# Performance work log

Measured on AMD Instinct MI355X. Metric: run time of the kernel, lower is better.

## Reference

```python
import jax, jax.numpy as jnp
import numpy as np

N, E, F_IN, E_DIM, H, T, L = 20000, 160000, 64, 32, 100, 5, 2
F_T = H // T  # per-tower output = 20

# PNAConv degree histogram -> average log-degree scalar (constant w.r.t. grads)
DEG_HIST = np.array([7,54,215,574,1147,1835,2447,2797,2797,2486,1989,1446,964,593,339,181,136], dtype=np.float64)
_bins = np.arange(len(DEG_HIST), dtype=np.float64)
AVG_LOG = np.float32((np.log(_bins + 1.0) * DEG_HIST).sum() / DEG_HIST.sum())


def _segment_stats(m, dst, n):
    # m: [E, T, H] messages; returns count [N] and [N, T, 4H] (mean|min|max|std)
    ones = jnp.ones((m.shape[0],), m.dtype)
    cnt = jax.ops.segment_sum(ones, dst, n)
    c = jnp.maximum(cnt, 1.0)[:, None, None]
    mean = jax.ops.segment_sum(m, dst, n) / c
    mean2 = jax.ops.segment_sum(m * m, dst, n) / c
    std = jnp.sqrt(jnp.maximum(mean2 - mean * mean, 0.0) + 1e-5)
    has = (cnt > 0)[:, None, None]
    mn = jnp.where(has, jax.ops.segment_min(m, dst, n), 0.0)
    mx = jnp.where(has, jax.ops.segment_max(m, dst, n), 0.0)
    return cnt, jnp.concatenate([mean, mn, mx, std], -1)


def _pna_conv(x, ea, src, dst, eeW, eeb, preW, preb, postW, postb, linW, linb):
    # x: [N, H] nodes, ea: [E, H] embedded edge attrs
    n = x.shape[0]
    e = ea.shape[0]
    xt = jnp.broadcast_to(x[:, None, :], (n, T, H))            # divide_input=False: repeat per tower
    e_enc = ea @ eeW + eeb                                     # edge_encoder [E, H]
    e_t = jnp.broadcast_to(e_enc[:, None, :], (e, T, H))
    h = jnp.concatenate([xt[dst], xt[src], e_t], -1)           # message cat [x_i, x_j, edge] -> [E, T, 3H]
    m = jnp.einsum('etf,tfh->eth', h, preW) + preb             # per-tower pre-MLP (1 layer) -> [E, T, H]
    cnt, agg = _segment_stats(m, dst, n)                       # [N, T, 4H]
    amp = (jnp.log(jnp.maximum(cnt, 1.0) + 1.0) / AVG_LOG)[:, None, None]
    scaled = jnp.concatenate([agg, agg * amp, agg / amp], -1)  # identity|amplification|attenuation -> [N, T, 12H]
    out = jnp.concatenate([xt, scaled], -1)                    # [N, T, 13H]
    out = jnp.einsum('ntf,tfo->nto', out, postW) + postb       # per-tower post-MLP -> [N, T, H/T]
    return out.reshape(n, H) @ linW + linb


def reference(x, edge_attr, node_emb_W, node_emb_b, edge_emb_W, edge_emb_b,
              ee_W, ee_b, pre_W, pre_b, post_W, post_b, lin_W, lin_b,
              bn_gamma, bn_beta, em_W1, em_b1, em_W2, em_b2,
              mlp_W1, mlp_b1, mlp_W2, mlp_b2, mlp_W3, mlp_b3, edge_index):
    src, dst = edge_index[0], edge_index[1]
    h = x @ node_emb_W + node_emb_b
    ea = edge_attr @ edge_emb_W + edge_emb_b
    for l in range(L):
        c = _pna_conv(h, ea, src, dst, ee_W[l], ee_b[l], pre_W[l], pre_b[l],
                      post_W[l], post_b[l], lin_W[l], lin_b[l])
        mu = c.mean(0)
        var = jnp.mean((c - mu) ** 2, 0)                       # BatchNorm (batch stats, biased var)
        h = jax.nn.relu(bn_gamma[l] * (c - mu) * jax.lax.rsqrt(var + 1e-5) + bn_beta[l])
        z = jnp.concatenate([h[src], h[dst], ea], -1)          # edge-update MLP
        ea = jax.nn.relu(z @ em_W1[l] + em_b1[l]) @ em_W2[l] + em_b2[l]
    o = jnp.concatenate([jax.nn.relu(h[src]), jax.nn.relu(h[dst]), ea], -1)
    o = jax.nn.relu(o @ mlp_W1 + mlp_b1)
    o = jax.nn.relu(o @ mlp_W2 + mlp_b2)
    return o @ mlp_W3 + mlp_b3                                 # [E, 1] per-edge logits


def setup_inputs() -> dict:
    key = jax.random.key(0)
    ks = iter(jax.random.split(key, 40))
    g = lambda shape, fan: jax.random.normal(next(ks), shape, jnp.float32) / np.float32(np.sqrt(fan))
    return {
        'x': jax.random.normal(next(ks), (N, F_IN), jnp.float32),
        'edge_attr': jax.random.normal(next(ks), (E, E_DIM), jnp.float32),
        'node_emb_W': g((F_IN, H), F_IN), 'node_emb_b': jnp.zeros((H,), jnp.float32),
        'edge_emb_W': g((E_DIM, H), E_DIM), 'edge_emb_b': jnp.zeros((H,), jnp.float32),
        'ee_W': g((L, H, H), H), 'ee_b': jnp.zeros((L, H), jnp.float32),
        'pre_W': g((L, T, 3 * H, H), 3 * H), 'pre_b': jnp.zeros((L, T, H), jnp.float32),
        'post_W': g((L, T, 13 * H, F_T), 13 * H), 'post_b': jnp.zeros((L, T, F_T), jnp.float32),
        'lin_W': g((L, H, H), H), 'lin_b': jnp.zeros((L, H), jnp.float32),
        'bn_gamma': jnp.ones((L, H), jnp.float32), 'bn_beta': jnp.zeros((L, H), jnp.float32),
        'em_W1': g((L, 3 * H, H), 3 * H), 'em_b1': jnp.zeros((L, H), jnp.float32),
        'em_W2': g((L, H, H), H), 'em_b2': jnp.zeros((L, H), jnp.float32),
        'mlp_W1': g((3 * H, 50), 3 * H), 'mlp_b1': jnp.zeros((50,), jnp.float32),
        'mlp_W2': g((50, 25), 50), 'mlp_b2': jnp.zeros((25,), jnp.float32),
        'mlp_W3': g((25, 1), 25), 'mlp_b3': jnp.zeros((1,), jnp.float32),
        'edge_index': jax.random.randint(next(ks), (2, E), 0, N, dtype=jnp.int32),
    }
```

## Files before the change

### kernel.cpp

```cpp
#include <hip/hip_runtime.h>
#include <cmath>

#define NN 20000
#define EE 160000
#define HH 100
#define TT 5
#define FT 20
#define LL 2
#define FIN 64
#define EDIM 32
#define CN 2500
#define NCH 8
#define CAP 23040

typedef __attribute__((ext_vector_type(8))) short bf16x8;
typedef __attribute__((ext_vector_type(4))) float f32x4;

__device__ inline float bf2f(unsigned short u) {
    union { unsigned i; float f; } x; x.i = ((unsigned)u) << 16; return x.f;
}
__device__ inline unsigned short f2bf(float f) {
    union { float f; unsigned i; } x; x.f = f;
    unsigned r = x.i + 0x7fff + ((x.i >> 16) & 1);
    return (unsigned short)(r >> 16);
}
__device__ inline unsigned packsplit(float v) {
    unsigned short hi = f2bf(v);
    float rem = v - bf2f(hi);
    unsigned short lo = f2bf(rem);
    return ((unsigned)hi << 16) | lo;
}

__global__ void hist_kernel(const int* __restrict__ edst, int* __restrict__ counts) {
    int e = blockIdx.x * 256 + threadIdx.x;
    if (e < EE) atomicAdd(&counts[edst[e]], 1);
}

__global__ __launch_bounds__(1024) void scan_kernel(const int* __restrict__ counts,
                                                    int* __restrict__ row_ptr,
                                                    int* __restrict__ fillp) {
    __shared__ int part[1024];
    int tid = threadIdx.x;
    const int PER = 20;
    int base = tid * PER;
    int s = 0;
    for (int i = 0; i < PER; ++i) {
        int idx = base + i;
        if (idx < NN) s += counts[idx];
    }
    part[tid] = s;
    __syncthreads();
    for (int off = 1; off < 1024; off <<= 1) {
        int v = (tid >= off) ? part[tid - off] : 0;
        __syncthreads();
        part[tid] += v;
        __syncthreads();
    }
    int run = (tid == 0) ? 0 : part[tid - 1];
    for (int i = 0; i < PER; ++i) {
        int idx = base + i;
        if (idx < NN) {
            row_ptr[idx] = run;
            fillp[idx] = run;
            run += counts[idx];
        }
    }
    if (tid == 1023) row_ptr[NN] = run;
}

__global__ void fill_kernel(const int* __restrict__ edst, int* __restrict__ fillp,
                            int* __restrict__ esorted) {
    int e = blockIdx.x * 256 + threadIdx.x;
    if (e < EE) {
        int pos = atomicAdd(&fillp[edst[e]], 1);
        esorted[pos] = e;
    }
}

__global__ void pack_kernel(const float* __restrict__ src, unsigned* __restrict__ dst, int n) {
    int i = blockIdx.x * 256 + threadIdx.x;
    if (i < n) dst[i] = packsplit(src[i]);
}

__global__ void repack_preW(const float* __restrict__ preW_l, float* __restrict__ Bcat) {
    int idx = blockIdx.x * 256 + threadIdx.x;
    if (idx >= 300 * 500) return;
    int k = idx / 500, n = idx % 500;
    int t = n / 100, hc = n % 100;
    Bcat[idx] = preW_l[(t * 300 + k) * 100 + hc];
}

__global__ void comb_kernel(const float* __restrict__ Bcat, const float* __restrict__ eeW,
                            const float* __restrict__ eeb, const float* __restrict__ preb,
                            float* __restrict__ Bcomb, float* __restrict__ biasc) {
    int idx = blockIdx.x * 256 + threadIdx.x;
    if (idx < 50000) {
        int i = idx / 500, n = idx % 500;
        float acc = 0.f;
        for (int j = 0; j < 100; ++j) acc += eeW[i * 100 + j] * Bcat[(200 + j) * 500 + n];
        Bcomb[idx] = acc;
    } else if (idx < 50500) {
        int n = idx - 50000;
        float acc = preb[n];
        for (int j = 0; j < 100; ++j) acc += eeb[j] * Bcat[(200 + j) * 500 + n];
        biasc[n] = acc;
    }
}

__global__ void pack_BT(const float* __restrict__ src, unsigned* __restrict__ dst,
                        int Kuse, int Nsrc, int koff, int total) {
    int idx = blockIdx.x * 256 + threadIdx.x;
    if (idx >= total) return;
    int n = idx >> 7, k = idx & 127;
    float v = (k < Kuse && n < Nsrc) ? src[(size_t)(koff + k) * Nsrc + n] : 0.f;
    dst[idx] = packsplit(v);
}

__global__ void pack_Wx(const float* __restrict__ postW, unsigned* __restrict__ dst) {
    int idx = blockIdx.x * 256 + threadIdx.x;
    if (idx >= 128 * 128) return;
    int col = idx >> 7, k = idx & 127;
    float v = 0.f;
    if (col < 100 && k < 100) {
        int t = col / 20, o = col % 20;
        v = postW[((size_t)t * 1300 + k) * 20 + o];
    }
    dst[idx] = packsplit(v);
}

__global__ void pack_Wpost(const float* __restrict__ postW, unsigned* __restrict__ dst) {
    int idx = blockIdx.x * 256 + threadIdx.x;
    int t = blockIdx.y;
    if (idx >= 128 * 512) return;
    int col = idx >> 9, k = idx & 511;
    float v = 0.f;
    if (col < 60 && k < 400) {
        int gg = col / 20, o = col % 20;
        v = postW[((size_t)t * 1300 + 100 + gg * 400 + k) * 20 + o];
    }
    dst[(size_t)t * 128 * 512 + idx] = packsplit(v);
}

template<int MODE, int NSLICE>
__global__ __launch_bounds__(512) void gemm_mfma(
    const unsigned* __restrict__ A_pk, int lda, int Kv,
    const unsigned* __restrict__ Bt_pk, int ldb,
    float* __restrict__ C, unsigned* __restrict__ Cpk,
    const float* __restrict__ bias, int ldc,
    const int* __restrict__ esorted, const int* __restrict__ row_ptr, int nbase,
    const int* __restrict__ esrc, const int* __restrict__ edst,
    const float* __restrict__ V1, const float* __restrict__ V2,
    const float* __restrict__ V3, const float* __restrict__ b1v,
    int M, int N, int sAz, int sBz, int sCz)
{
    __shared__ unsigned short sAh[128 * 64], sAl[128 * 64];
    __shared__ unsigned short sBh[128 * 64], sBl[128 * 64];
    int tid = threadIdx.x;
    int row0 = blockIdx.x * 128;
    int col0 = blockIdx.y * 128;
    if (MODE == 3) {
        A_pk  += (size_t)blockIdx.z * sAz;
        Bt_pk += (size_t)blockIdx.z * sBz;
        C     += (size_t)blockIdx.z * sCz;
    }

    int Me = M, pbeg = 0;
    if (MODE == 1) {
        pbeg = row_ptr[nbase];
        int ned = row_ptr[nbase + CN] - pbeg;
        Me = ned < M ? ned : M;
    }
    if (row0 >= Me) return;

    int lane = tid & 63, wid = tid >> 6;
    int wr = wid >> 2, wc = wid & 3;
    int llo = lane & 15, lhi = lane >> 4;
    f32x4 acc[4][2] = {};

    for (int sl = 0; sl < NSLICE; ++sl) {
        int kbase = sl * 64;
        if (sl) __syncthreads();
        for (int t = tid; t < 2048; t += 512) {
            int col = t >> 4, q = t & 15, k0 = q * 4;
            int kg = kbase + k0;
            uint4 p = make_uint4(0u, 0u, 0u, 0u);
            if (kg < Kv || NSLICE * 64 <= ldb)
                p = *(const uint4*)(Bt_pk + ((size_t)(col0 + col) * ldb + kg));
            unsigned h0 = __builtin_amdgcn_perm(p.y, p.x, 0x07060302u);
            unsigned h1 = __builtin_amdgcn_perm(p.w, p.z, 0x07060302u);
            unsigned l0 = __builtin_amdgcn_perm(p.y, p.x, 0x05040100u);
            unsigned l1 = __builtin_amdgcn_perm(p.w, p.z, 0x05040100u);
            int byte = (col * 128 + k0 * 2) ^ ((col & 7) << 4);
            *(uint2*)((char*)sBh + byte) = make_uint2(h0, h1);
            *(uint2*)((char*)sBl + byte) = make_uint2(l0, l1);
        }
        for (int t = tid; t < 2048; t += 512) {
            int r = t >> 4, q = t & 15, k0 = q * 4;
            int rg = row0 + r;
            int kg = kbase + k0;
            uint4 p = make_uint4(0u, 0u, 0u, 0u);
            if (MODE == 2) {
                if (rg < Me && kg < Kv) {
                    int s = esrc[rg], d = edst[rg];
                    float4 a = *(const float4*)(V1 + (size_t)s * 100 + kg);
                    float4 b = *(const float4*)(V2 + (size_t)d * 100 + kg);
                    float4 c = *(const float4*)(V3 + (size_t)rg * 100 + kg);
                    float4 bb = *(const float4*)(b1v + kg);
                    p.x = packsplit(fmaxf(a.x + b.x + c.x + bb.x, 0.f));
                    p.y = packsplit(fmaxf(a.y + b.y + c.y + bb.y, 0.f));
                    p.z = packsplit(fmaxf(a.z + b.z + c.z + bb.z, 0.f));
                    p.w = packsplit(fmaxf(a.w + b.w + c.w + bb.w, 0.f));
                }
            } else {
                if (rg < Me && kg < Kv) {
                    int ra = rg;
                    if (MODE == 1) ra = esorted[pbeg + rg];
                    p = *(const uint4*)(A_pk + (size_t)ra * lda + kg);
                }
            }
            unsigned h0 = __builtin_amdgcn_perm(p.y, p.x, 0x07060302u);
            unsigned h1 = __builtin_amdgcn_perm(p.w, p.z, 0x07060302u);
            unsigned l0 = __builtin_amdgcn_perm(p.y, p.x, 0x05040100u);
            unsigned l1 = __builtin_amdgcn_perm(p.w, p.z, 0x05040100u);
            int byte = (r * 128 + k0 * 2) ^ ((r & 7) << 4);
            *(uint2*)((char*)sAh + byte) = make_uint2(h0, h1);
            *(uint2*)((char*)sAl + byte) = make_uint2(l0, l1);
        }
        __syncthreads();

#pragma unroll
        for (int ks = 0; ks < 2; ++ks) {
            bf16x8 ah[4], al[4], bh[2], bl[2];
            int kb = ks * 64 + lhi * 16;
#pragma unroll
            for (int i = 0; i < 4; ++i) {
                int r = wr * 64 + i * 16 + llo;
                int byte = (r * 128 + kb) ^ ((r & 7) << 4);
                ah[i] = *(const bf16x8*)((const char*)sAh + byte);
                al[i] = *(const bf16x8*)((const char*)sAl + byte);
            }
#pragma unroll
            for (int j = 0; j < 2; ++j) {
                int c = wc * 32 + j * 16 + llo;
                int byte = (c * 128 + kb) ^ ((c & 7) << 4);
                bh[j] = *(const bf16x8*)((const char*)sBh + byte);
                bl[j] = *(const bf16x8*)((const char*)sBl + byte);
            }
#pragma unroll
            for (int i = 0; i < 4; ++i)
#pragma unroll
                for (int j = 0; j < 2; ++j) {
                    acc[i][j] = __builtin_amdgcn_mfma_f32_16x16x32_bf16(ah[i], bh[j], acc[i][j], 0, 0, 0);
                    acc[i][j] = __builtin_amdgcn_mfma_f32_16x16x32_bf16(ah[i], bl[j], acc[i][j], 0, 0, 0);
                    acc[i][j] = __builtin_amdgcn_mfma_f32_16x16x32_bf16(al[i], bh[j], acc[i][j], 0, 0, 0);
                }
        }
    }
#pragma unroll
    for (int j = 0; j < 2; ++j) {
        int cg = col0 + wc * 32 + j * 16 + llo;
        if (cg >= N) continue;
        float bb = bias ? bias[cg] : 0.f;
#pragma unroll
        for (int i = 0; i < 4; ++i)
#pragma unroll
            for (int rr = 0; rr < 4; ++rr) {
                int rg = row0 + wr * 64 + i * 16 + lhi * 4 + rr;
                if (rg < Me) {
                    float v = acc[i][j][rr] + bb;
                    if (Cpk) Cpk[(size_t)rg * ldc + cg] = packsplit(v);
                    else     C[(size_t)rg * ldc + cg] = v;
                }
            }
    }
}

__global__ __launch_bounds__(256) void stats_lite(const float* __restrict__ U1c,
                                                  const float* __restrict__ U2,
                                                  const float* __restrict__ U3s,
                                                  const float* __restrict__ biasc,
                                                  const int* __restrict__ row_ptr,
                                                  const int* __restrict__ esorted,
                                                  const int* __restrict__ esrc,
                                                  int nbase, float avg_log,
                                                  unsigned* __restrict__ A_pk,
                                                  float* __restrict__ amp_arr) {
    __shared__ int sS[4][96];
    int tid = threadIdx.x;
    int g = tid >> 6, l = tid & 63;
    int nloc = blockIdx.x * 4 + g;
    int node = nbase + nloc;
    int pbeg_c = row_ptr[nbase];
    int pbegG = row_ptr[node], pendG = row_ptr[node + 1];
    int pbeg = pbegG - pbeg_c; if (pbeg > CAP) pbeg = CAP;
    int pend = pendG - pbeg_c; if (pend > CAP) pend = CAP;
    int deg = pend - pbeg; if (deg < 0) deg = 0; if (deg > 96) deg = 96;
    if (l < deg) sS[g][l] = esrc[esorted[pbegG + l]];
    if (l + 64 < deg) sS[g][l + 64] = esrc[esorted[pbegG + l + 64]];
    if (l == 0) amp_arr[node] = logf((float)(deg > 0 ? deg : 1) + 1.f) / avg_log;
    __syncthreads();
    float rdeg = 1.f / (float)(deg > 0 ? deg : 1);
    float sq_eps = sqrtf(1e-5f);
    for (int cb = l; cb < 125; cb += 64) {
        int c4 = cb * 4;
        float4 u1 = *(const float4*)(U1c + (size_t)nloc * 500 + c4);
        float4 bc = *(const float4*)(biasc + c4);
        float bx = u1.x + bc.x, by = u1.y + bc.y, bz = u1.z + bc.z, bw = u1.w + bc.w;
        float s0x = 0.f, s0y = 0.f, s0z = 0.f, s0w = 0.f;
        float q0x = 0.f, q0y = 0.f, q0z = 0.f, q0w = 0.f;
        float mnx = 3.4e38f, mny = 3.4e38f, mnz = 3.4e38f, mnw = 3.4e38f;
        float mxx = -3.4e38f, mxy = -3.4e38f, mxz = -3.4e38f, mxw = -3.4e38f;
#pragma unroll 2
        for (int i = 0; i < deg; ++i) {
            float4 a = *(const float4*)(U3s + (size_t)(pbeg + i) * 500 + c4);
            float4 b = *(const float4*)(U2 + (size_t)sS[g][i] * 500 + c4);
            float vx = a.x + b.x;
            float vy = a.y + b.y;
            float vz = a.z + b.z;
            float vw = a.w + b.w;
            s0x += vx; s0y += vy; s0z += vz; s0w += vw;
            q0x += vx * vx; q0y += vy * vy; q0z += vz * vz; q0w += vw * vw;
            mnx = fminf(mnx, vx); mny = fminf(mny, vy); mnz = fminf(mnz, vz); mnw = fminf(mnw, vw);
            mxx = fmaxf(mxx, vx); mxy = fmaxf(mxy, vy); mxz = fmaxf(mxz, vz); mxw = fmaxf(mxw, vw);
        }
        float m0x = s0x * rdeg, m0y = s0y * rdeg, m0z = s0z * rdeg, m0w = s0w * rdeg;
        uint4 ome, omn, omx, osd;
        if (deg == 0) {
            unsigned z = 0u, se = packsplit(sq_eps);
            ome = make_uint4(z, z, z, z);
            omn = make_uint4(z, z, z, z);
            omx = make_uint4(z, z, z, z);
            osd = make_uint4(se, se, se, se);
        } else {
            float sdx = sqrtf(fmaxf(q0x * rdeg - m0x * m0x, 0.f) + 1e-5f);
            float sdy = sqrtf(fmaxf(q0y * rdeg - m0y * m0y, 0.f) + 1e-5f);
            float sdz = sqrtf(fmaxf(q0z * rdeg - m0z * m0z, 0.f) + 1e-5f);
            float sdw = sqrtf(fmaxf(q0w * rdeg - m0w * m0w, 0.f) + 1e-5f);
            ome = make_uint4(packsplit(m0x + bx), packsplit(m0y + by), packsplit(m0z + bz), packsplit(m0w + bw));
            omn = make_uint4(packsplit(mnx + bx), packsplit(mny + by), packsplit(mnz + bz), packsplit(mnw + bw));
            omx = make_uint4(packsplit(mxx + bx), packsplit(mxy + by), packsplit(mxz + bz), packsplit(mxw + bw));
            osd = make_uint4(packsplit(sdx), packsplit(sdy), packsplit(sdz), packsplit(sdw));
        }
        int t = c4 / 100, hh = c4 % 100;
        unsigned* base = A_pk + ((size_t)t * CN + nloc) * 400 + hh;
        *(uint4*)(base +   0) = ome;
        *(uint4*)(base + 100) = omn;
        *(uint4*)(base + 200) = omx;
        *(uint4*)(base + 300) = osd;
    }
}

__global__ void combine_kernel(const float* __restrict__ Gx, const float* __restrict__ G,
                               const float* __restrict__ amp_arr, const float* __restrict__ postb,
                               int nbase, unsigned* __restrict__ cpre_pk) {
    int idx = blockIdx.x * 256 + threadIdx.x;
    if (idx >= CN * 128) return;
    int nloc = idx >> 7, c = idx & 127;
    int node = nbase + nloc;
    if (c >= 100) { cpre_pk[(size_t)node * 128 + c] = 0u; return; }
    int t = c / 20, o = c % 20;
    float a = amp_arr[node], inv = 1.f / a;
    const float* Gt = G + ((size_t)t * CN + nloc) * 64;
    float v = Gx[(size_t)node * 128 + c] + Gt[o] + a * Gt[20 + o] + inv * Gt[40 + o] + postb[c];
    cpre_pk[(size_t)node * 128 + c] = packsplit(v);
}

__global__ __launch_bounds__(128) void bn_reduce(const float* __restrict__ c, float* __restrict__ bnbuf) {
    int j = threadIdx.x;
    if (j >= 100) return;
    int r0 = blockIdx.x * 250;
    float s = 0.f, s2 = 0.f;
    for (int r = r0; r < r0 + 250; ++r) {
        float v = c[(size_t)r * 100 + j];
        s += v; s2 += v * v;
    }
    atomicAdd(&bnbuf[j], s);
    atomicAdd(&bnbuf[100 + j], s2);
}

__global__ void bn_apply2(const float* __restrict__ c, const float* __restrict__ bnbuf,
                          const float* __restrict__ gamma, const float* __restrict__ beta,
                          unsigned* __restrict__ h_pk) {
    int idx = blockIdx.x * 256 + threadIdx.x;
    if (idx >= NN * 100) return;
    int j = idx % 100;
    float mu = bnbuf[j] * (1.f / NN);
    float var = bnbuf[100 + j] * (1.f / NN) - mu * mu;
    float inv = rsqrtf(var + 1e-5f);
    float v = gamma[j] * (c[idx] - mu) * inv + beta[j];
    h_pk[idx] = packsplit(fmaxf(v, 0.f));
}

__global__ __launch_bounds__(256) void final_fused(const float* __restrict__ P1,
                                                   const float* __restrict__ P2,
                                                   const float* __restrict__ Q,
                                                   const int* __restrict__ esrc,
                                                   const int* __restrict__ edst,
                                                   const float* __restrict__ b1,
                                                   const float* __restrict__ W2,
                                                   const float* __restrict__ b2,
                                                   const float* __restrict__ W3,
                                                   const float* __restrict__ b3,
                                                   float* __restrict__ out) {
    __shared__ float sW2[50 * 25], sW3[25], sb1[50], sb2[25];
    __shared__ float sO1[32][52];
    __shared__ float sO2[32][26];
    __shared__ int sS[32], sD[32];
    int tid = threadIdx.x;
    int e0 = blockIdx.x * 32;
    for (int i = tid; i < 1250; i += 256) sW2[i] = W2[i];
    if (tid < 25) { sW3[tid] = W3[tid]; sb2[tid] = b2[tid]; }
    if (tid < 50) sb1[tid] = b1[tid];
    if (tid < 32) { sS[tid] = esrc[e0 + tid]; sD[tid] = edst[e0 + tid]; }
    __syncthreads();
    for (int idx = tid; idx < 1600; idx += 256) {
        int r = idx / 50, j = idx % 50;
        float v = P1[(size_t)sS[r] * 50 + j] + P2[(size_t)sD[r] * 50 + j]
                + Q[(size_t)(e0 + r) * 50 + j] + sb1[j];
        sO1[r][j] = fmaxf(v, 0.f);
    }
    __syncthreads();
    for (int idx = tid; idx < 800; idx += 256) {
        int r = idx / 25, j = idx % 25;
        float acc = sb2[j];
        for (int k = 0; k < 50; ++k) acc += sO1[r][k] * sW2[k * 25 + j];
        sO2[r][j] = fmaxf(acc, 0.f);
    }
    __syncthreads();
    if (tid < 32) {
        float acc = b3[0];
        for (int k = 0; k < 25; ++k) acc += sO2[tid][k] * sW3[k];
        out[e0 + tid] = acc;
    }
}

extern "C" void kernel_launch(void* const* d_in, const int* in_sizes, int n_in,
                              void* d_out, int out_size, void* d_ws, size_t ws_size,
                              hipStream_t stream) {
    (void)in_sizes; (void)n_in; (void)out_size; (void)ws_size;
    const float* x          = (const float*)d_in[0];
    const float* edge_attr  = (const float*)d_in[1];
    const float* node_emb_W = (const float*)d_in[2];
    const float* node_emb_b = (const float*)d_in[3];
    const float* edge_emb_W = (const float*)d_in[4];
    const float* edge_emb_b = (const float*)d_in[5];
    const float* ee_W       = (const float*)d_in[6];
    const float* ee_b       = (const float*)d_in[7];
    const float* pre_W      = (const float*)d_in[8];
    const float* pre_b      = (const float*)d_in[9];
    const float* post_W     = (const float*)d_in[10];
    const float* post_b     = (const float*)d_in[11];
    const float* lin_W      = (const float*)d_in[12];
    const float* lin_b      = (const float*)d_in[13];
    const float* bn_gamma   = (const float*)d_in[14];
    const float* bn_beta    = (const float*)d_in[15];
    const float* em_W1      = (const float*)d_in[16];
    const float* em_b1      = (const float*)d_in[17];
    const float* em_W2      = (const float*)d_in[18];
    const float* em_b2      = (const float*)d_in[19];
    const float* mlp_W1     = (const float*)d_in[20];
    const float* mlp_b1     = (const float*)d_in[21];
    const float* mlp_W2     = (const float*)d_in[22];
    const float* mlp_b2     = (const float*)d_in[23];
    const float* mlp_W3     = (const float*)d_in[24];
    const float* mlp_b3     = (const float*)d_in[25];
    const int*   edge_index = (const int*)d_in[26];
    const int* esrc = edge_index;
    const int* edst = edge_index + EE;

    static const double deg_hist[17] = {7, 54, 215, 574, 1147, 1835, 2447, 2797, 2797,
                                        2486, 1989, 1446, 964, 593, 339, 181, 136};
    double num = 0.0, den = 0.0;
    for (int i = 0; i < 17; ++i) { num += log((double)i + 1.0) * deg_hist[i]; den += deg_hist[i]; }
    float avg_log = (float)(num / den);

    float* f = (float*)d_ws;
    unsigned* h_pk    = (unsigned*)f;  f += (size_t)NN * 100;
    float*    cbuf    = f;             f += (size_t)NN * 100;
    float*    V2      = f;             f += (size_t)NN * 100;
    unsigned* ea_pk   = (unsigned*)f;  f += (size_t)EE * 100;
    float*    U1c     = f;             f += (size_t)CN * 500;
    float*    P1      = f;             f += (size_t)NN * 50;
    float*    P2      = f;             f += (size_t)NN * 50;
    float*    Gx      = f;             f += (size_t)NN * 128;
    unsigned* cpre_pk = (unsigned*)f;  f += (size_t)NN * 128;
    float*    amp_arr = f;             f += (size_t)NN;
    float*    Gbuf    = f;             f += (size_t)TT * CN * 64;
    float*    arena   = f;             f += (size_t)21600000;
    float*    Bcat    = f;             f += 300 * 500;
    float*    Bcomb   = f;             f += 100 * 500;
    float*    biasc   = f;             f += 512;
    float*    bnbuf   = f;             f += 256;
    unsigned* B1t     = (unsigned*)f;  f += 512 * 128;
    unsigned* B2t     = (unsigned*)f;  f += 512 * 128;
    unsigned* B3t     = (unsigned*)f;  f += 512 * 128;
    unsigned* nembt   = (unsigned*)f;  f += 128 * 128;
    unsigned* eembt   = (unsigned*)f;  f += 128 * 128;
    unsigned* W1at    = (unsigned*)f;  f += 128 * 128;
    unsigned* W1bt    = (unsigned*)f;  f += 128 * 128;
    unsigned* W1ct    = (unsigned*)f;  f += 128 * 128;
    unsigned* W2t     = (unsigned*)f;  f += 128 * 128;
    unsigned* M1at    = (unsigned*)f;  f += 128 * 128;
    unsigned* M1bt    = (unsigned*)f;  f += 128 * 128;
    unsigned* M1ct    = (unsigned*)f;  f += 128 * 128;
    unsigned* Wx_pk   = (unsigned*)f;  f += 128 * 128;
    unsigned* Wpost_pk= (unsigned*)f;  f += (size_t)TT * 128 * 512;
    unsigned* linWt   = (unsigned*)f;  f += 128 * 128;
    int* counts  = (int*)f;            f += NN;
    int* row_ptr = (int*)f;            f += NN + 1;
    int* fillp   = (int*)f;            f += NN;
    int* esorted = (int*)f;            f += EE;
    unsigned* A_pk = (unsigned*)f;     f += (size_t)TT * CN * 400;

    unsigned* eattr_pk = (unsigned*)arena;
    unsigned* x_pk     = (unsigned*)(arena + 5200000);
    float*    U2       = arena;
    float*    U3s      = arena + 10000000;
    float*    V3       = arena;
    float*    Q        = arena;
    float*    V1       = cbuf;

    hipMemsetAsync(counts, 0, NN * sizeof(int), stream);
    hist_kernel<<<(EE + 255) / 256, 256, 0, stream>>>(edst, counts);
    scan_kernel<<<1, 1024, 0, stream>>>(counts, row_ptr, fillp);
    fill_kernel<<<(EE + 255) / 256, 256, 0, stream>>>(edst, fillp, esorted);

    pack_kernel<<<(NN * FIN + 255) / 256, 256, 0, stream>>>(x, x_pk, NN * FIN);
    pack_kernel<<<(EE * EDIM + 255) / 256, 256, 0, stream>>>(edge_attr, eattr_pk, EE * EDIM);
    pack_BT<<<64, 256, 0, stream>>>(node_emb_W, nembt, FIN, HH, 0, 128 * 128);
    pack_BT<<<64, 256, 0, stream>>>(edge_emb_W, eembt, EDIM, HH, 0, 128 * 128);
    gemm_mfma<0, 1><<<dim3(157, 1), 512, 0, stream>>>(
        x_pk, FIN, FIN, nembt, 128, nullptr, h_pk, node_emb_b, 100,
        nullptr, nullptr, 0, nullptr, nullptr, nullptr, nullptr, nullptr, nullptr, NN, 100, 0, 0, 0);
    gemm_mfma<0, 1><<<dim3(1250, 1), 512, 0, stream>>>(
        eattr_pk, EDIM, EDIM, eembt, 128, nullptr, ea_pk, edge_emb_b, 100,
        nullptr, nullptr, 0, nullptr, nullptr, nullptr, nullptr, nullptr, nullptr, EE, 100, 0, 0, 0);

    for (int l = 0; l < LL; ++l) {
        repack_preW<<<(150000 + 255) / 256, 256, 0, stream>>>(pre_W + (size_t)l * TT * 300 * HH, Bcat);
        comb_kernel<<<(50500 + 255) / 256, 256, 0, stream>>>(Bcat, ee_W + (size_t)l * HH * HH,
                                                             ee_b + l * HH, pre_b + l * TT * HH,
                                                             Bcomb, biasc);
        pack_BT<<<256, 256, 0, stream>>>(Bcat, B1t, 100, 500, 0, 512 * 128);
        pack_BT<<<256, 256, 0, stream>>>(Bcat, B2t, 100, 500, 100, 512 * 128);
        pack_BT<<<256, 256, 0, stream>>>(Bcomb, B3t, 100, 500, 0, 512 * 128);
        const float* W1l = em_W1 + (size_t)l * 300 * HH;
        pack_BT<<<64, 256, 0, stream>>>(W1l, W1at, 100, 100, 0, 128 * 128);
        pack_BT<<<64, 256, 0, stream>>>(W1l, W1bt, 100, 100, 100, 128 * 128);
        pack_BT<<<64, 256, 0, stream>>>(W1l, W1ct, 100, 100, 200, 128 * 128);
        pack_BT<<<64, 256, 0, stream>>>(em_W2 + (size_t)l * HH * HH, W2t, 100, 100, 0, 128 * 128);
        const float* postWl = post_W + (size_t)l * TT * 1300 * FT;
        pack_Wx<<<64, 256, 0, stream>>>(postWl, Wx_pk);
        pack_Wpost<<<dim3(256, TT), 256, 0, stream>>>(postWl, Wpost_pk);
        pack_BT<<<64, 256, 0, stream>>>(lin_W + (size_t)l * HH * HH, linWt, 100, 100, 0, 128 * 128);

        gemm_mfma<0, 2><<<dim3(157, 4), 512, 0, stream>>>(
            h_pk, 100, 100, B2t, 128, U2, nullptr, nullptr, 500,
            nullptr, nullptr, 0, nullptr, nullptr, nullptr, nullptr, nullptr, nullptr, NN, 500, 0, 0, 0);
        gemm_mfma<0, 2><<<dim3(157, 1), 512, 0, stream>>>(
            h_pk, 100, 100, Wx_pk, 128, Gx, nullptr, nullptr, 128,
            nullptr, nullptr, 0, nullptr, nullptr, nullptr, nullptr, nullptr, nullptr, NN, 100, 0, 0, 0);

        for (int c = 0; c < NCH; ++c) {
            int nbase = c * CN;
            gemm_mfma<0, 2><<<dim3(20, 4), 512, 0, stream>>>(
                h_pk + (size_t)nbase * 100, 100, 100, B1t, 128, U1c, nullptr, nullptr, 500,
                nullptr, nullptr, 0, nullptr, nullptr, nullptr, nullptr, nullptr, nullptr, CN, 500, 0, 0, 0);
            gemm_mfma<1, 2><<<dim3(CAP / 128, 4), 512, 0, stream>>>(
                ea_pk, 100, 100, B3t, 128, U3s, nullptr, nullptr, 500,
                esorted, row_ptr, nbase, nullptr, nullptr, nullptr, nullptr, nullptr, nullptr,
                CAP, 500, 0, 0, 0);
            stats_lite<<<CN / 4, 256, 0, stream>>>(U1c, U2, U3s, biasc, row_ptr, esorted, esrc,
                                                   nbase, avg_log, A_pk, amp_arr);
            gemm_mfma<3, 7><<<dim3(20, 1, TT), 512, 0, stream>>>(
                A_pk, 400, 400, Wpost_pk, 512, Gbuf, nullptr, nullptr, 64,
                nullptr, nullptr, 0, nullptr, nullptr, nullptr, nullptr, nullptr, nullptr,
                CN, 60, CN * 400, 128 * 512, CN * 64);
            combine_kernel<<<(CN * 128 + 255) / 256, 256, 0, stream>>>(
                Gx, Gbuf, amp_arr, post_b + l * TT * FT, nbase, cpre_pk);
        }
        gemm_mfma<0, 2><<<dim3(157, 1), 512, 0, stream>>>(
            cpre_pk, 128, 128, linWt, 128, cbuf, nullptr, lin_b + l * HH, 100,
            nullptr, nullptr, 0, nullptr, nullptr, nullptr, nullptr, nullptr, nullptr, NN, 100, 0, 0, 0);
        hipMemsetAsync(bnbuf, 0, 256 * sizeof(float), stream);
        bn_reduce<<<80, 128, 0, stream>>>(cbuf, bnbuf);
        bn_apply2<<<(NN * 100 + 255) / 256, 256, 0, stream>>>(cbuf, bnbuf,
                                                              bn_gamma + l * HH, bn_beta + l * HH,
                                                              h_pk);
        gemm_mfma<0, 2><<<dim3(157, 1), 512, 0, stream>>>(
            h_pk, 100, 100, W1at, 128, V1, nullptr, nullptr, 100,
            nullptr, nullptr, 0, nullptr, nullptr, nullptr, nullptr, nullptr, nullptr, NN, 100, 0, 0, 0);
        gemm_mfma<0, 2><<<dim3(157, 1), 512, 0, stream>>>(
            h_pk, 100, 100, W1bt, 128, V2, nullptr, nullptr, 100,
            nullptr, nullptr, 0, nullptr, nullptr, nullptr, nullptr, nullptr, nullptr, NN, 100, 0, 0, 0);
        gemm_mfma<0, 2><<<dim3(1250, 1), 512, 0, stream>>>(
            ea_pk, 100, 100, W1ct, 128, V3, nullptr, nullptr, 100,
            nullptr, nullptr, 0, nullptr, nullptr, nullptr, nullptr, nullptr, nullptr, EE, 100, 0, 0, 0);
        gemm_mfma<2, 2><<<dim3(1250, 1), 512, 0, stream>>>(
            nullptr, 100, 100, W2t, 128, nullptr, ea_pk, em_b2 + l * HH, 100,
            nullptr, nullptr, 0, esrc, edst, V1, V2, V3, em_b1 + l * HH, EE, 100, 0, 0, 0);
    }

    pack_BT<<<64, 256, 0, stream>>>(mlp_W1, M1at, 100, 50, 0, 128 * 128);
    pack_BT<<<64, 256, 0, stream>>>(mlp_W1, M1bt, 100, 50, 100, 128 * 128);
    pack_BT<<<64, 256, 0, stream>>>(mlp_W1, M1ct, 100, 50, 200, 128 * 128);
    gemm_mfma<0, 2><<<dim3(157, 1), 512, 0, stream>>>(
        h_pk, 100, 100, M1at, 128, P1, nullptr, nullptr, 50,
        nullptr, nullptr, 0, nullptr, nullptr, nullptr, nullptr, nullptr, nullptr, NN, 50, 0, 0, 0);
    gemm_mfma<0, 2><<<dim3(157, 1), 512, 0, stream>>>(
        h_pk, 100, 100, M1bt, 128, P2, nullptr, nullptr, 50,
        nullptr, nullptr, 0, nullptr, nullptr, nullptr, nullptr, nullptr, nullptr, NN, 50, 0, 0, 0);
    gemm_mfma<0, 2><<<dim3(1250, 1), 512, 0, stream>>>(
        ea_pk, 100, 100, M1ct, 128, Q, nullptr, nullptr, 50,
        nullptr, nullptr, 0, nullptr, nullptr, nullptr, nullptr, nullptr, nullptr, EE, 50, 0, 0, 0);
    final_fused<<<EE / 32, 256, 0, stream>>>(P1, P2, Q, esrc, edst,
                                             mlp_b1, mlp_W2, mlp_b2, mlp_W3, mlp_b3,
                                             (float*)d_out);
}
```

Measured before the change: 2.642 ms.

## Store intermediate GEMM outputs as bf16 and hoist U1 GEMM out of chunk loop

Adds an output-mode template parameter so GEMMs can write plain bf16 instead of fp32 or split-packed values. The U1/U2/U3 tables feeding the per-node statistics kernel and the V1/V2/V3 tables feeding the edge MLP are now stored as bf16, halving the bytes moved by the bandwidth-bound gather loops. The per-chunk U1 GEMM becomes one full-size GEMM before the chunk loop, and the workspace arena shrinks. This costs precision, since the intermediate messages are rounded to bf16 before the sum, min, max and std aggregation.

```diff
diff --git a/kernel.cpp b/kernel.cpp
--- a/kernel.cpp
+++ b/kernel.cpp
@@ -141,7 +141,7 @@
     dst[(size_t)t * 128 * 512 + idx] = packsplit(v);
 }
 
-template<int MODE, int NSLICE>
+template<int MODE, int NSLICE, int OUT>
 __global__ __launch_bounds__(512) void gemm_mfma(
     const unsigned* __restrict__ A_pk, int lda, int Kv,
     const unsigned* __restrict__ Bt_pk, int ldb,
@@ -149,8 +149,8 @@
     const float* __restrict__ bias, int ldc,
     const int* __restrict__ esorted, const int* __restrict__ row_ptr, int nbase,
     const int* __restrict__ esrc, const int* __restrict__ edst,
-    const float* __restrict__ V1, const float* __restrict__ V2,
-    const float* __restrict__ V3, const float* __restrict__ b1v,
+    const unsigned short* __restrict__ V1, const unsigned short* __restrict__ V2,
+    const unsigned short* __restrict__ V3, const float* __restrict__ b1v,
     int M, int N, int sAz, int sBz, int sCz)
 {
     __shared__ unsigned short sAh[128 * 64], sAl[128 * 64];
@@ -202,14 +202,14 @@
             if (MODE == 2) {
                 if (rg < Me && kg < Kv) {
                     int s = esrc[rg], d = edst[rg];
-                    float4 a = *(const float4*)(V1 + (size_t)s * 100 + kg);
-                    float4 b = *(const float4*)(V2 + (size_t)d * 100 + kg);
-                    float4 c = *(const float4*)(V3 + (size_t)rg * 100 + kg);
+                    ushort4 a4 = *(const ushort4*)(V1 + (size_t)s * 100 + kg);
+                    ushort4 b4 = *(const ushort4*)(V2 + (size_t)d * 100 + kg);
+                    ushort4 c4 = *(const ushort4*)(V3 + (size_t)rg * 100 + kg);
                     float4 bb = *(const float4*)(b1v + kg);
-                    p.x = packsplit(fmaxf(a.x + b.x + c.x + bb.x, 0.f));
-                    p.y = packsplit(fmaxf(a.y + b.y + c.y + bb.y, 0.f));
-                    p.z = packsplit(fmaxf(a.z + b.z + c.z + bb.z, 0.f));
-                    p.w = packsplit(fmaxf(a.w + b.w + c.w + bb.w, 0.f));
+                    p.x = packsplit(fmaxf(bf2f(a4.x) + bf2f(b4.x) + bf2f(c4.x) + bb.x, 0.f));
+                    p.y = packsplit(fmaxf(bf2f(a4.y) + bf2f(b4.y) + bf2f(c4.y) + bb.y, 0.f));
+                    p.z = packsplit(fmaxf(bf2f(a4.z) + bf2f(b4.z) + bf2f(c4.z) + bb.z, 0.f));
+                    p.w = packsplit(fmaxf(bf2f(a4.w) + bf2f(b4.w) + bf2f(c4.w) + bb.w, 0.f));
                 }
             } else {
                 if (rg < Me && kg < Kv) {
@@ -268,16 +268,17 @@
                 int rg = row0 + wr * 64 + i * 16 + lhi * 4 + rr;
                 if (rg < Me) {
                     float v = acc[i][j][rr] + bb;
-                    if (Cpk) Cpk[(size_t)rg * ldc + cg] = packsplit(v);
-                    else     C[(size_t)rg * ldc + cg] = v;
+                    if (OUT == 1)      Cpk[(size_t)rg * ldc + cg] = packsplit(v);
+                    else if (OUT == 2) ((unsigned short*)Cpk)[(size_t)rg * ldc + cg] = f2bf(v);
+                    else               C[(size_t)rg * ldc + cg] = v;
                 }
             }
     }
 }
 
-__global__ __launch_bounds__(256) void stats_lite(const float* __restrict__ U1c,
-                                                  const float* __restrict__ U2,
-                                                  const float* __restrict__ U3s,
+__global__ __launch_bounds__(256) void stats_lite(const unsigned short* __restrict__ U1b,
+                                                  const unsigned short* __restrict__ U2b,
+                                                  const unsigned short* __restrict__ U3b,
                                                   const float* __restrict__ biasc,
                                                   const int* __restrict__ row_ptr,
                                                   const int* __restrict__ esorted,
@@ -303,21 +304,22 @@
     float sq_eps = sqrtf(1e-5f);
     for (int cb = l; cb < 125; cb += 64) {
         int c4 = cb * 4;
-        float4 u1 = *(const float4*)(U1c + (size_t)nloc * 500 + c4);
+        ushort4 u1 = *(const ushort4*)(U1b + (size_t)node * 500 + c4);
         float4 bc = *(const float4*)(biasc + c4);
-        float bx = u1.x + bc.x, by = u1.y + bc.y, bz = u1.z + bc.z, bw = u1.w + bc.w;
+        float bx = bf2f(u1.x) + bc.x, by = bf2f(u1.y) + bc.y;
+        float bz = bf2f(u1.z) + bc.z, bw = bf2f(u1.w) + bc.w;
         float s0x = 0.f, s0y = 0.f, s0z = 0.f, s0w = 0.f;
         float q0x = 0.f, q0y = 0.f, q0z = 0.f, q0w = 0.f;
         float mnx = 3.4e38f, mny = 3.4e38f, mnz = 3.4e38f, mnw = 3.4e38f;
         float mxx = -3.4e38f, mxy = -3.4e38f, mxz = -3.4e38f, mxw = -3.4e38f;
 #pragma unroll 2
         for (int i = 0; i < deg; ++i) {
-            float4 a = *(const float4*)(U3s + (size_t)(pbeg + i) * 500 + c4);
-            float4 b = *(const float4*)(U2 + (size_t)sS[g][i] * 500 + c4);
-            float vx = a.x + b.x;
-            float vy = a.y + b.y;
-            float vz = a.z + b.z;
-            float vw = a.w + b.w;
+            ushort4 a = *(const ushort4*)(U3b + (size_t)(pbeg + i) * 500 + c4);
+            ushort4 b = *(const ushort4*)(U2b + (size_t)sS[g][i] * 500 + c4);
+            float vx = bf2f(a.x) + bf2f(b.x);
+            float vy = bf2f(a.y) + bf2f(b.y);
+            float vz = bf2f(a.z) + bf2f(b.z);
+            float vw = bf2f(a.w) + bf2f(b.w);
             s0x += vx; s0y += vy; s0z += vz; s0w += vw;
             q0x += vx * vx; q0y += vy * vy; q0z += vz * vz; q0w += vw * vw;
             mnx = fminf(mnx, vx); mny = fminf(mny, vy); mnz = fminf(mnz, vz); mnw = fminf(mnw, vw);
@@ -475,50 +477,50 @@
     float avg_log = (float)(num / den);
 
     float* f = (float*)d_ws;
-    unsigned* h_pk    = (unsigned*)f;  f += (size_t)NN * 100;
-    float*    cbuf    = f;             f += (size_t)NN * 100;
-    float*    V2      = f;             f += (size_t)NN * 100;
-    unsigned* ea_pk   = (unsigned*)f;  f += (size_t)EE * 100;
-    float*    U1c     = f;             f += (size_t)CN * 500;
-    float*    P1      = f;             f += (size_t)NN * 50;
-    float*    P2      = f;             f += (size_t)NN * 50;
-    float*    Gx      = f;             f += (size_t)NN * 128;
-    unsigned* cpre_pk = (unsigned*)f;  f += (size_t)NN * 128;
-    float*    amp_arr = f;             f += (size_t)NN;
-    float*    Gbuf    = f;             f += (size_t)TT * CN * 64;
-    float*    arena   = f;             f += (size_t)21600000;
-    float*    Bcat    = f;             f += 300 * 500;
-    float*    Bcomb   = f;             f += 100 * 500;
-    float*    biasc   = f;             f += 512;
-    float*    bnbuf   = f;             f += 256;
-    unsigned* B1t     = (unsigned*)f;  f += 512 * 128;
-    unsigned* B2t     = (unsigned*)f;  f += 512 * 128;
-    unsigned* B3t     = (unsigned*)f;  f += 512 * 128;
-    unsigned* nembt   = (unsigned*)f;  f += 128 * 128;
-    unsigned* eembt   = (unsigned*)f;  f += 128 * 128;
-    unsigned* W1at    = (unsigned*)f;  f += 128 * 128;
-    unsigned* W1bt    = (unsigned*)f;  f += 128 * 128;
-    unsigned* W1ct    = (unsigned*)f;  f += 128 * 128;
-    unsigned* W2t     = (unsigned*)f;  f += 128 * 128;
-    unsigned* M1at    = (unsigned*)f;  f += 128 * 128;
-    unsigned* M1bt    = (unsigned*)f;  f += 128 * 128;
-    unsigned* M1ct    = (unsigned*)f;  f += 128 * 128;
-    unsigned* Wx_pk   = (unsigned*)f;  f += 128 * 128;
-    unsigned* Wpost_pk= (unsigned*)f;  f += (size_t)TT * 128 * 512;
-    unsigned* linWt   = (unsigned*)f;  f += 128 * 128;
-    int* counts  = (int*)f;            f += NN;
-    int* row_ptr = (int*)f;            f += NN + 1;
-    int* fillp   = (int*)f;            f += NN;
-    int* esorted = (int*)f;            f += EE;
-    unsigned* A_pk = (unsigned*)f;     f += (size_t)TT * CN * 400;
+    unsigned* h_pk    = (unsigned*)f;       f += (size_t)NN * 100;
+    float*    cbuf    = f;                  f += (size_t)NN * 100;
+    unsigned short* V1b = (unsigned short*)f; f += (size_t)NN * 100 / 2;
+    unsigned short* V2b = (unsigned short*)f; f += (size_t)NN * 100 / 2;
+    unsigned* ea_pk   = (unsigned*)f;       f += (size_t)EE * 100;
+    unsigned short* U1b = (unsigned short*)f; f += (size_t)NN * 500 / 2;
+    float*    P1      = f;                  f += (size_t)NN * 50;
+    float*    P2      = f;                  f += (size_t)NN * 50;
+    float*    Gx      = f;                  f += (size_t)NN * 128;
+    unsigned* cpre_pk = (unsigned*)f;       f += (size_t)NN * 128;
+    float*    amp_arr = f;                  f += (size_t)NN;
+    float*    Gbuf    = f;                  f += (size_t)TT * CN * 64;
+    float*    arena   = f;                  f += (size_t)11200000;
+    float*    Bcat    = f;                  f += 300 * 500;
+    float*    Bcomb   = f;                  f += 100 * 500;
+    float*    biasc   = f;                  f += 512;
+    float*    bnbuf   = f;                  f += 256;
+    unsigned* B1t     = (unsigned*)f;       f += 512 * 128;
+    unsigned* B2t     = (unsigned*)f;       f += 512 * 128;
+    unsigned* B3t     = (unsigned*)f;       f += 512 * 128;
+    unsigned* nembt   = (unsigned*)f;       f += 128 * 128;
+    unsigned* eembt   = (unsigned*)f;       f += 128 * 128;
+    unsigned* W1at    = (unsigned*)f;       f += 128 * 128;
+    unsigned* W1bt    = (unsigned*)f;       f += 128 * 128;
+    unsigned* W1ct    = (unsigned*)f;       f += 128 * 128;
+    unsigned* W2t     = (unsigned*)f;       f += 128 * 128;
+    unsigned* M1at    = (unsigned*)f;       f += 128 * 128;
+    unsigned* M1bt    = (unsigned*)f;       f += 128 * 128;
+    unsigned* M1ct    = (unsigned*)f;       f += 128 * 128;
+    unsigned* Wx_pk   = (unsigned*)f;       f += 128 * 128;
+    unsigned* Wpost_pk= (unsigned*)f;       f += (size_t)TT * 128 * 512;
+    unsigned* linWt   = (unsigned*)f;       f += 128 * 128;
+    int* counts  = (int*)f;                 f += NN;
+    int* row_ptr = (int*)f;                 f += NN + 1;
+    int* fillp   = (int*)f;                 f += NN;
+    int* esorted = (int*)f;                 f += EE;
+    unsigned* A_pk = (unsigned*)f;          f += (size_t)TT * CN * 400;
 
     unsigned* eattr_pk = (unsigned*)arena;
     unsigned* x_pk     = (unsigned*)(arena + 5200000);
-    float*    U2       = arena;
-    float*    U3s      = arena + 10000000;
-    float*    V3       = arena;
+    unsigned short* U2b = (unsigned short*)arena;
+    unsigned short* U3b = (unsigned short*)(arena + 5250000);
+    unsigned short* V3b = (unsigned short*)arena;
     float*    Q        = arena;
-    float*    V1       = cbuf;
 
     hipMemsetAsync(counts, 0, NN * sizeof(int), stream);
     hist_kernel<<<(EE + 255) / 256, 256, 0, stream>>>(edst, counts);
@@ -529,10 +531,10 @@
     pack_kernel<<<(EE * EDIM + 255) / 256, 256, 0, stream>>>(edge_attr, eattr_pk, EE * EDIM);
     pack_BT<<<64, 256, 0, stream>>>(node_emb_W, nembt, FIN, HH, 0, 128 * 128);
     pack_BT<<<64, 256, 0, stream>>>(edge_emb_W, eembt, EDIM, HH, 0, 128 * 128);
-    gemm_mfma<0, 1><<<dim3(157, 1), 512, 0, stream>>>(
+    gemm_mfma<0, 1, 1><<<dim3(157, 1), 512, 0, stream>>>(
         x_pk, FIN, FIN, nembt, 128, nullptr, h_pk, node_emb_b, 100,
         nullptr, nullptr, 0, nullptr, nullptr, nullptr, nullptr, nullptr, nullptr, NN, 100, 0, 0, 0);
-    gemm_mfma<0, 1><<<dim3(1250, 1), 512, 0, stream>>>(
+    gemm_mfma<0, 1, 1><<<dim3(1250, 1), 512, 0, stream>>>(
         eattr_pk, EDIM, EDIM, eembt, 128, nullptr, ea_pk, edge_emb_b, 100,
         nullptr, nullptr, 0, nullptr, nullptr, nullptr, nullptr, nullptr, nullptr, EE, 100, 0, 0, 0);
 
@@ -554,32 +556,32 @@
         pack_Wpost<<<dim3(256, TT), 256, 0, stream>>>(postWl, Wpost_pk);
         pack_BT<<<64, 256, 0, stream>>>(lin_W + (size_t)l * HH * HH, linWt, 100, 100, 0, 128 * 128);
 
-        gemm_mfma<0, 2><<<dim3(157, 4), 512, 0, stream>>>(
-            h_pk, 100, 100, B2t, 128, U2, nullptr, nullptr, 500,
+        gemm_mfma<0, 2, 2><<<dim3(157, 4), 512, 0, stream>>>(
+            h_pk, 100, 100, B2t, 128, nullptr, (unsigned*)U2b, nullptr, 500,
             nullptr, nullptr, 0, nullptr, nullptr, nullptr, nullptr, nullptr, nullptr, NN, 500, 0, 0, 0);
-        gemm_mfma<0, 2><<<dim3(157, 1), 512, 0, stream>>>(
+        gemm_mfma<0, 2, 2><<<dim3(157, 4), 512, 0, stream>>>(
+            h_pk, 100, 100, B1t, 128, nullptr, (unsigned*)U1b, nullptr, 500,
+            nullptr, nullptr, 0, nullptr, nullptr, nullptr, nullptr, nullptr, nullptr, NN, 500, 0, 0, 0);
+        gemm_mfma<0, 2, 0><<<dim3(157, 1), 512, 0, stream>>>(
             h_pk, 100, 100, Wx_pk, 128, Gx, nullptr, nullptr, 128,
             nullptr, nullptr, 0, nullptr, nullptr, nullptr, nullptr, nullptr, nullptr, NN, 100, 0, 0, 0);
 
         for (int c = 0; c < NCH; ++c) {
             int nbase = c * CN;
-            gemm_mfma<0, 2><<<dim3(20, 4), 512, 0, stream>>>(
-                h_pk + (size_t)nbase * 100, 100, 100, B1t, 128, U1c, nullptr, nullptr, 500,
-                nullptr, nullptr, 0, nullptr, nullptr, nullptr, nullptr, nullptr, nullptr, CN, 500, 0, 0, 0);
-            gemm_mfma<1, 2><<<dim3(CAP / 128, 4), 512, 0, stream>>>(
-                ea_pk, 100, 100, B3t, 128, U3s, nullptr, nullptr, 500,
+            gemm_mfma<1, 2, 2><<<dim3(CAP / 128, 4), 512, 0, stream>>>(
+                ea_pk, 100, 100, B3t, 128, nullptr, (unsigned*)U3b, nullptr, 500,
                 esorted, row_ptr, nbase, nullptr, nullptr, nullptr, nullptr, nullptr, nullptr,
                 CAP, 500, 0, 0, 0);
-            stats_lite<<<CN / 4, 256, 0, stream>>>(U1c, U2, U3s, biasc, row_ptr, esorted, esrc,
+            stats_lite<<<CN / 4, 256, 0, stream>>>(U1b, U2b, U3b, biasc, row_ptr, esorted, esrc,
                                                    nbase, avg_log, A_pk, amp_arr);
-            gemm_mfma<3, 7><<<dim3(20, 1, TT), 512, 0, stream>>>(
+            gemm_mfma<3, 7, 0><<<dim3(20, 1, TT), 512, 0, stream>>>(
                 A_pk, 400, 400, Wpost_pk, 512, Gbuf, nullptr, nullptr, 64,
                 nullptr, nullptr, 0, nullptr, nullptr, nullptr, nullptr, nullptr, nullptr,
                 CN, 60, CN * 400, 128 * 512, CN * 64);
             combine_kernel<<<(CN * 128 + 255) / 256, 256, 0, stream>>>(
                 Gx, Gbuf, amp_arr, post_b + l * TT * FT, nbase, cpre_pk);
         }
-        gemm_mfma<0, 2><<<dim3(157, 1), 512, 0, stream>>>(
+        gemm_mfma<0, 2, 0><<<dim3(157, 1), 512, 0, stream>>>(
             cpre_pk, 128, 128, linWt, 128, cbuf, nullptr, lin_b + l * HH, 100,
             nullptr, nullptr, 0, nullptr, nullptr, nullptr, nullptr, nullptr, nullptr, NN, 100, 0, 0, 0);
         hipMemsetAsync(bnbuf, 0, 256 * sizeof(float), stream);
@@ -587,30 +589,30 @@
         bn_apply2<<<(NN * 100 + 255) / 256, 256, 0, stream>>>(cbuf, bnbuf,
                                                               bn_gamma + l * HH, bn_beta + l * HH,
                                                               h_pk);
-        gemm_mfma<0, 2><<<dim3(157, 1), 512, 0, stream>>>(
-            h_pk, 100, 100, W1at, 128, V1, nullptr, nullptr, 100,
+        gemm_mfma<0, 2, 2><<<dim3(157, 1), 512, 0, stream>>>(
+            h_pk, 100, 100, W1at, 128, nullptr, (unsigned*)V1b, nullptr, 100,
             nullptr, nullptr, 0, nullptr, nullptr, nullptr, nullptr, nullptr, nullptr, NN, 100, 0, 0, 0);
-        gemm_mfma<0, 2><<<dim3(157, 1), 512, 0, stream>>>(
-            h_pk, 100, 100, W1bt, 128, V2, nullptr, nullptr, 100,
+        gemm_mfma<0, 2, 2><<<dim3(157, 1), 512, 0, stream>>>(
+            h_pk, 100, 100, W1bt, 128, nullptr, (unsigned*)V2b, nullptr, 100,
             nullptr, nullptr, 0, nullptr, nullptr, nullptr, nullptr, nullptr, nullptr, NN, 100, 0, 0, 0);
-        gemm_mfma<0, 2><<<dim3(1250, 1), 512, 0, stream>>>(
-            ea_pk, 100, 100, W1ct, 128, V3, nullptr, nullptr, 100,
+        gemm_mfma<0, 2, 2><<<dim3(1250, 1), 512, 0, stream>>>(
+            ea_pk, 100, 100, W1ct, 128, nullptr, (unsigned*)V3b, nullptr, 100,
             nullptr, nullptr, 0, nullptr, nullptr, nullptr, nullptr, nullptr, nullptr, EE, 100, 0, 0, 0);
-        gemm_mfma<2, 2><<<dim3(1250, 1), 512, 0, stream>>>(
+        gemm_mfma<2, 2, 1><<<dim3(1250, 1), 512, 0, stream>>>(
             nullptr, 100, 100, W2t, 128, nullptr, ea_pk, em_b2 + l * HH, 100,
-            nullptr, nullptr, 0, esrc, edst, V1, V2, V3, em_b1 + l * HH, EE, 100, 0, 0, 0);
+            nullptr, nullptr, 0, esrc, edst, V1b, V2b, V3b, em_b1 + l * HH, EE, 100, 0, 0, 0);
     }
 
     pack_BT<<<64, 256, 0, stream>>>(mlp_W1, M1at, 100, 50, 0, 128 * 128);
     pack_BT<<<64, 256, 0, stream>>>(mlp_W1, M1bt, 100, 50, 100, 128 * 128);
     pack_BT<<<64, 256, 0, stream>>>(mlp_W1, M1ct, 100, 50, 200, 128 * 128);
-    gemm_mfma<0, 2><<<dim3(157, 1), 512, 0, stream>>>(
+    gemm_mfma<0, 2, 0><<<dim3(157, 1), 512, 0, stream>>>(
         h_pk, 100, 100, M1at, 128, P1, nullptr, nullptr, 50,
         nullptr, nullptr, 0, nullptr, nullptr, nullptr, nullptr, nullptr, nullptr, NN, 50, 0, 0, 0);
-    gemm_mfma<0, 2><<<dim3(157, 1), 512, 0, stream>>>(
+    gemm_mfma<0, 2, 0><<<dim3(157, 1), 512, 0, stream>>>(
         h_pk, 100, 100, M1bt, 128, P2, nullptr, nullptr, 50,
         nullptr, nullptr, 0, nullptr, nullptr, nullptr, nullptr, nullptr, nullptr, NN, 50, 0, 0, 0);
-    gemm_mfma<0, 2><<<dim3(1250, 1), 512, 0, stream>>>(
+    gemm_mfma<0, 2, 0><<<dim3(1250, 1), 512, 0, stream>>>(
         ea_pk, 100, 100, M1ct, 128, Q, nullptr, nullptr, 50,
         nullptr, nullptr, 0, nullptr, nullptr, nullptr, nullptr, nullptr, nullptr, EE, 50, 0, 0, 0);
     final_fused<<<EE / 32, 256, 0, stream>>>(P1, P2, Q, esrc, edst,
```

Result: faster. 2.267 ms (-14.2%).
